# Kernel tuning notes

Measured on AMD Instinct MI355X. Metric: run time of the kernel, lower is better.

Reference implementation:

```python
import jax, jax.numpy as jnp
import numpy as np

NUM_HEADS = 16
ROPE_BASE = 10000.0


def _rope(q, k, seq_len, head_dim):
    # cos/sin: [S, D] -> broadcast over batch and heads via [:, None, :]
    inv_freq = 1.0 / (ROPE_BASE ** (jnp.arange(0, head_dim, 2, dtype=jnp.float32) / head_dim))
    t = jnp.arange(seq_len, dtype=jnp.float32)
    freqs = t[:, None] * inv_freq[None, :]            # [S, D/2]
    emb = jnp.concatenate((freqs, freqs), axis=-1)    # [S, D]
    cos = jnp.cos(emb)[:, None, :]                    # [S, 1, D]
    sin = jnp.sin(emb)[:, None, :]
    def rot(x):
        return jnp.stack([-x[..., 1::2], x[..., ::2]], axis=-1).reshape(x.shape)
    q = q * cos + rot(q) * sin
    k = k * cos + rot(k) * sin
    return q, k


def setup_inputs() -> dict:
    key = jax.random.key(0)
    ks = jax.random.split(key, 5)
    B, S, D = 2, 2048, 2048
    return {
        "hidden_states": jax.random.normal(ks[0], (B, S, D), dtype=jnp.float32),
        "Wq": jax.random.normal(ks[1], (D, D), dtype=jnp.float32) * 0.02,
        "Wk": jax.random.normal(ks[2], (D, D), dtype=jnp.float32) * 0.02,
        "Wv": jax.random.normal(ks[3], (D, D), dtype=jnp.float32) * 0.02,
        "Wo": jax.random.normal(ks[4], (D, D), dtype=jnp.float32) * 0.02,
        "attention_mask": jnp.ones((B, S), dtype=bool),
        "position_ids": S,  # passed to rotary as seq_len
    }


def reference(hidden_states, Wq, Wk, Wv, Wo, attention_mask, position_ids):
    B, S, D = hidden_states.shape
    H = NUM_HEADS
    hd = D // H
    q = (hidden_states @ Wq.T).reshape(B, S, H, hd)
    k = (hidden_states @ Wk.T).reshape(B, S, H, hd)
    v = (hidden_states @ Wv.T).reshape(B, S, H, hd)
    q, k = _rope(q, k, position_ids, hd)
    scores = jnp.einsum('bqhd,bkhd->bhqk', q, k) / jnp.sqrt(jnp.float32(hd))
    scores = jnp.where(attention_mask[:, None, None, :], scores, -jnp.inf)
    attn = jax.nn.softmax(scores, axis=-1)
    out = jnp.einsum('bhqk,bkhd->bqhd', attn, v).reshape(B, S, D)
    return out @ Wo.T
```

## Files before the change

kernel.cpp:

```cpp
#include <hip/hip_runtime.h>
#include <hip/hip_bf16.h>
#include <math.h>

typedef __hip_bfloat16 bf16;
typedef __attribute__((ext_vector_type(8))) short bf16x8;
typedef __attribute__((ext_vector_type(4))) float f32x4;

#define AS1 __attribute__((address_space(1)))
#define AS3 __attribute__((address_space(3)))

static constexpr int BATCH = 2, S = 2048, D = 2048, H = 16, HD = 128;
static constexpr int M = BATCH * S;
static constexpr float SCALE = 0.08838834764831845f;

__device__ __forceinline__ void gload_lds16(const void* g, void* l) {
  __builtin_amdgcn_global_load_lds((AS1 void*)g, (AS3 void*)l, 16, 0, 0);
}

__device__ __forceinline__ unsigned short f2bu(float f) {
  bf16 h = __float2bfloat16(f);
  return *reinterpret_cast<unsigned short*>(&h);
}

__global__ void cast_kernel(const float* __restrict__ in,
                            unsigned short* __restrict__ out, int n4) {
  int i = blockIdx.x * blockDim.x + threadIdx.x;
  int stride = gridDim.x * blockDim.x;
  for (; i < n4; i += stride) {
    float4 v = reinterpret_cast<const float4*>(in)[i];
    ushort4 o;
    o.x = f2bu(v.x); o.y = f2bu(v.y); o.z = f2bu(v.z); o.w = f2bu(v.w);
    reinterpret_cast<ushort4*>(out)[i] = o;
  }
}

__global__ void rope_tab_kernel(float2* __restrict__ cs) {
  int s = blockIdx.x, j = threadIdx.x;
  double inv = exp(-(double)j * 0.14391156831212793);
  float ang = (float)s * (float)inv;
  double da = (double)ang;
  cs[s * 64 + j] = make_float2((float)cos(da), (float)sin(da));
}

template <int EPI>
__global__ __launch_bounds__(256, 2) void gemm_bt(const bf16* __restrict__ A,
                                                  const bf16* __restrict__ B,
                                                  void* __restrict__ outp,
                                                  const float2* __restrict__ cs,
                                                  float oscale) {
  constexpr int K = 2048;
  __shared__ bf16 smA[2][128 * 32];
  __shared__ bf16 smB[2][128 * 32];
  const int tid = threadIdx.x;
  const int l = tid & 63, w = tid >> 6;
  const int wm = w >> 1, wn = w & 1;
  const int bm = blockIdx.y, bn = blockIdx.x;
  const int lr = l & 15, lg = l >> 4;

  f32x4 acc[4][4] = {};

  auto stage = [&](bf16* dst, const bf16* src, int row0, int k0) {
    #pragma unroll
    for (int i = 0; i < 2; ++i) {
      int idx = tid + i * 256;
      int row = idx >> 2, seg = idx & 3;
      gload_lds16(src + (size_t)(row0 + row) * K + k0 + seg * 8, dst + idx * 8);
    }
  };

  stage(smA[0], A, bm * 128, 0);
  stage(smB[0], B, bn * 128, 0);
  asm volatile("s_waitcnt vmcnt(0)" ::: "memory");
  __syncthreads();

  for (int kt = 0; kt < K / 32; ++kt) {
    const int cur = kt & 1;
    if (kt + 1 < K / 32) {
      stage(smA[cur ^ 1], A, bm * 128, (kt + 1) * 32);
      stage(smB[cur ^ 1], B, bn * 128, (kt + 1) * 32);
    }
    bf16x8 af[4], bfr[4];
    #pragma unroll
    for (int fm = 0; fm < 4; ++fm)
      af[fm] = *reinterpret_cast<const bf16x8*>(
          &smA[cur][(wm * 64 + fm * 16 + lr) * 32 + lg * 8]);
    #pragma unroll
    for (int fn = 0; fn < 4; ++fn)
      bfr[fn] = *reinterpret_cast<const bf16x8*>(
          &smB[cur][(wn * 64 + fn * 16 + lr) * 32 + lg * 8]);
    #pragma unroll
    for (int fm = 0; fm < 4; ++fm)
      #pragma unroll
      for (int fn = 0; fn < 4; ++fn)
        acc[fm][fn] = __builtin_amdgcn_mfma_f32_16x16x32_bf16(af[fm], bfr[fn],
                                                              acc[fm][fn], 0, 0, 0);
    __syncthreads();
  }

  const int row0 = bm * 128 + wm * 64 + lg * 4;
  const int col0 = bn * 128 + wn * 64 + lr;

  if constexpr (EPI == 0) {
    bf16* o = reinterpret_cast<bf16*>(outp);
    #pragma unroll
    for (int fm = 0; fm < 4; ++fm) {
      #pragma unroll
      for (int fn = 0; fn < 4; ++fn) {
        const int col = col0 + fn * 16;
        const int j = col & 63;
        const bool odd = (col & 1);
        #pragma unroll
        for (int r = 0; r < 4; ++r) {
          float v = acc[fm][fn][r];
          float p = __shfl_xor(v, 1);
          int row = row0 + fm * 16 + r;
          int s = row & (S - 1);
          float2 c = cs[s * 64 + j];
          float nv = (v * c.x + (odd ? p : -p) * c.y) * oscale;
          o[(size_t)row * D + col] = __float2bfloat16(nv);
        }
      }
    }
  } else if constexpr (EPI == 1) {
    bf16* o = reinterpret_cast<bf16*>(outp);
    #pragma unroll
    for (int fm = 0; fm < 4; ++fm) {
      #pragma unroll
      for (int fn = 0; fn < 4; ++fn) {
        int row = row0 + fm * 16;
        int col = col0 + fn * 16;
        int b_ = row >> 11, sp = row & (S - 1);
        int h = col >> 7, d = col & (HD - 1);
        size_t off = ((size_t)(b_ * H + h) * HD + d) * S + sp;
        ushort4 pk;
        pk.x = f2bu(acc[fm][fn][0]);
        pk.y = f2bu(acc[fm][fn][1]);
        pk.z = f2bu(acc[fm][fn][2]);
        pk.w = f2bu(acc[fm][fn][3]);
        *reinterpret_cast<ushort4*>(o + off) = pk;
      }
    }
  } else {
    float* o = reinterpret_cast<float*>(outp);
    #pragma unroll
    for (int fm = 0; fm < 4; ++fm)
      #pragma unroll
      for (int fn = 0; fn < 4; ++fn)
        #pragma unroll
        for (int r = 0; r < 4; ++r)
          o[(size_t)(row0 + fm * 16 + r) * D + col0 + fn * 16] = acc[fm][fn][r];
  }
}

__global__ __launch_bounds__(256, 2) void attn_kernel(const bf16* __restrict__ Q,
                                                      const bf16* __restrict__ Kmat,
                                                      const bf16* __restrict__ Vt,
                                                      bf16* __restrict__ O) {
  __shared__ bf16 kv_lds[2][16384];
  __shared__ bf16 plds[4][16][72];
  const int tid = threadIdx.x;
  const int l = tid & 63, w = tid >> 6;
  const int lr = l & 15, lg = l >> 4;
  const int bh = blockIdx.y;
  const int b = bh >> 4, h = bh & 15;
  const int q0 = blockIdx.x * 64 + w * 16;

  bf16x8 aq[4];
  #pragma unroll
  for (int ks = 0; ks < 4; ++ks)
    aq[ks] = *reinterpret_cast<const bf16x8*>(
        &Q[((size_t)b * S + q0 + lr) * D + h * HD + ks * 32 + lg * 8]);

  const bf16* ksrc[4];
  const bf16* vsrc[4];
  int kldsoff[4], vldsoff[4];
  #pragma unroll
  for (int i = 0; i < 4; ++i) {
    int idx = tid + i * 256;
    int krow = idx >> 4, kcb = (idx & 15) << 4;
    int kcol = (kcb ^ ((krow & 7) << 4)) >> 1;
    ksrc[i] = Kmat + ((size_t)b * S + krow) * D + h * HD + kcol;
    kldsoff[i] = idx * 8;
    int vrow = idx >> 3, vcb = (idx & 7) << 4;
    int vcol = (vcb ^ ((vrow & 7) << 4)) >> 1;
    vsrc[i] = Vt + ((size_t)bh * HD + vrow) * S + vcol;
    vldsoff[i] = 8192 + idx * 8;
  }

  auto stage = [&](int buf, int t) {
    #pragma unroll
    for (int i = 0; i < 4; ++i) {
      gload_lds16(ksrc[i] + (size_t)t * 64 * D, &kv_lds[buf][kldsoff[i]]);
      gload_lds16(vsrc[i] + t * 64, &kv_lds[buf][vldsoff[i]]);
    }
  };

  f32x4 oacc[8] = {};
  float m[4], ls[4];
  #pragma unroll
  for (int r = 0; r < 4; ++r) { m[r] = -1e30f; ls[r] = 0.f; }

  stage(0, 0);
  asm volatile("s_waitcnt vmcnt(0)" ::: "memory");
  __syncthreads();

  const int swz = (lr & 7) << 4;

  for (int t = 0; t < S / 64; ++t) {
    const int cur = t & 1;
    if (t + 1 < S / 64) stage(cur ^ 1, t + 1);
    const bf16* Kl = &kv_lds[cur][0];
    const bf16* Vl = &kv_lds[cur][8192];

    f32x4 sf[4] = {};
    __builtin_amdgcn_s_setprio(1);
    #pragma unroll
    for (int ksub = 0; ksub < 4; ++ksub) {
      #pragma unroll
      for (int ks = 0; ks < 4; ++ks) {
        bf16x8 bk = *reinterpret_cast<const bf16x8*>(
            &Kl[(ksub * 16 + lr) * 128 + (((ks * 64 + lg * 16) ^ swz) >> 1)]);
        sf[ksub] = __builtin_amdgcn_mfma_f32_16x16x32_bf16(aq[ks], bk, sf[ksub], 0, 0, 0);
      }
    }
    __builtin_amdgcn_s_setprio(0);

    #pragma unroll
    for (int r = 0; r < 4; ++r) {
      float mx = fmaxf(fmaxf(sf[0][r], sf[1][r]), fmaxf(sf[2][r], sf[3][r]));
      #pragma unroll
      for (int off = 1; off < 16; off <<= 1) mx = fmaxf(mx, __shfl_xor(mx, off));
      if (!__all(mx <= m[r] + 8.f)) {
        float mn = fmaxf(m[r], mx);
        float al = __expf(m[r] - mn);
        m[r] = mn;
        ls[r] *= al;
        #pragma unroll
        for (int df = 0; df < 8; ++df) oacc[df][r] *= al;
      }
      #pragma unroll
      for (int ksub = 0; ksub < 4; ++ksub) {
        float p = __expf(sf[ksub][r] - m[r]);
        ls[r] += p;
        plds[w][lg * 4 + r][ksub * 16 + lr] = __float2bfloat16(p);
      }
    }

    bf16x8 pa0 = *reinterpret_cast<const bf16x8*>(&plds[w][lr][lg * 8]);
    bf16x8 pa1 = *reinterpret_cast<const bf16x8*>(&plds[w][lr][32 + lg * 8]);
    __builtin_amdgcn_s_setprio(1);
    #pragma unroll
    for (int df = 0; df < 8; ++df) {
      const int vr = df * 16 + lr;
      bf16x8 bv0 = *reinterpret_cast<const bf16x8*>(
          &Vl[vr * 64 + (((lg * 16) ^ swz) >> 1)]);
      bf16x8 bv1 = *reinterpret_cast<const bf16x8*>(
          &Vl[vr * 64 + (((64 + lg * 16) ^ swz) >> 1)]);
      oacc[df] = __builtin_amdgcn_mfma_f32_16x16x32_bf16(pa0, bv0, oacc[df], 0, 0, 0);
      oacc[df] = __builtin_amdgcn_mfma_f32_16x16x32_bf16(pa1, bv1, oacc[df], 0, 0, 0);
    }
    __builtin_amdgcn_s_setprio(0);
    asm volatile("s_waitcnt vmcnt(0)" ::: "memory");
    __syncthreads();
  }

  #pragma unroll
  for (int r = 0; r < 4; ++r) {
    #pragma unroll
    for (int off = 1; off < 16; off <<= 1) ls[r] += __shfl_xor(ls[r], off);
    ls[r] = 1.0f / ls[r];
  }
  #pragma unroll
  for (int df = 0; df < 8; ++df) {
    #pragma unroll
    for (int r = 0; r < 4; ++r) {
      float v = oacc[df][r] * ls[r];
      O[((size_t)b * S + q0 + lg * 4 + r) * D + h * HD + df * 16 + lr] =
          __float2bfloat16(v);
    }
  }
}

extern "C" void kernel_launch(void* const* d_in, const int* in_sizes, int n_in,
                              void* d_out, int out_size, void* d_ws, size_t ws_size,
                              hipStream_t stream) {
  const float* hs = (const float*)d_in[0];
  const float* Wq = (const float*)d_in[1];
  const float* Wk = (const float*)d_in[2];
  const float* Wv = (const float*)d_in[3];
  const float* Wo = (const float*)d_in[4];
  float* out = (float*)d_out;

  const size_t nTok = (size_t)M * D;
  const size_t nW = (size_t)D * D;
  bf16* hsb = (bf16*)d_ws;
  bf16* wqb = hsb + nTok;
  bf16* wkb = wqb + nW;
  bf16* wvb = wkb + nW;
  bf16* wob = wvb + nW;
  bf16* qb  = wob + nW;
  bf16* kb  = qb + nTok;
  bf16* vtb = kb + nTok;
  bf16* ob  = vtb + nTok;
  float2* cs = (float2*)(ob + nTok);

  cast_kernel<<<2048, 256, 0, stream>>>(hs, (unsigned short*)hsb, (int)(nTok / 4));
  cast_kernel<<<1024, 256, 0, stream>>>(Wq, (unsigned short*)wqb, (int)(nW / 4));
  cast_kernel<<<1024, 256, 0, stream>>>(Wk, (unsigned short*)wkb, (int)(nW / 4));
  cast_kernel<<<1024, 256, 0, stream>>>(Wv, (unsigned short*)wvb, (int)(nW / 4));
  cast_kernel<<<1024, 256, 0, stream>>>(Wo, (unsigned short*)wob, (int)(nW / 4));
  rope_tab_kernel<<<S, 64, 0, stream>>>(cs);

  dim3 gg(D / 128, M / 128);
  gemm_bt<0><<<gg, 256, 0, stream>>>(hsb, wqb, qb, cs, SCALE);
  gemm_bt<0><<<gg, 256, 0, stream>>>(hsb, wkb, kb, cs, 1.0f);
  gemm_bt<1><<<gg, 256, 0, stream>>>(hsb, wvb, vtb, nullptr, 1.0f);

  attn_kernel<<<dim3(S / 64, BATCH * H), 256, 0, stream>>>(qb, kb, vtb, ob);

  gemm_bt<2><<<gg, 256, 0, stream>>>(ob, wob, out, nullptr, 1.0f);
}
```

Baseline: 499.4 us.

## Process 32 query rows per wave in attention and restructure K/V staging

Each wave now handles two 16-row query tiles, and each block covers 128 queries. K and V fragments loaded from LDS are therefore reused across twice as many MFMAs, and half as many blocks reload the same K/V tiles. The LDS plan changes to double-buffered K with a single V buffer. V for the current tile is issued first and waited on with a partial vmcnt before the PV stage, so the V load overlaps the QK and softmax work. The max-rescale check is merged into one wave vote across both tiles, which cuts shuffles. The cost is higher register pressure under launch_bounds(256,2) and fewer blocks in the grid (512), which may reduce occupancy or cause spills.

Measured after the change: 440.0 us. -11.9%, faster.

```diff
diff --git a/kernel.cpp b/kernel.cpp
--- a/kernel.cpp
+++ b/kernel.cpp
@@ -156,51 +156,48 @@
                                                       const bf16* __restrict__ Kmat,
                                                       const bf16* __restrict__ Vt,
                                                       bf16* __restrict__ O) {
-  __shared__ bf16 kv_lds[2][16384];
-  __shared__ bf16 plds[4][16][72];
+  __shared__ bf16 kv_lds[24576];
+  __shared__ bf16 plds[4][32][72];
   const int tid = threadIdx.x;
   const int l = tid & 63, w = tid >> 6;
   const int lr = l & 15, lg = l >> 4;
   const int bh = blockIdx.y;
   const int b = bh >> 4, h = bh & 15;
-  const int q0 = blockIdx.x * 64 + w * 16;
-
-  bf16x8 aq[4];
-  #pragma unroll
-  for (int ks = 0; ks < 4; ++ks)
-    aq[ks] = *reinterpret_cast<const bf16x8*>(
-        &Q[((size_t)b * S + q0 + lr) * D + h * HD + ks * 32 + lg * 8]);
+  const int q0 = blockIdx.x * 128 + w * 32;
+
+  bf16x8 aq[2][4];
+  #pragma unroll
+  for (int qs = 0; qs < 2; ++qs)
+    #pragma unroll
+    for (int ks = 0; ks < 4; ++ks)
+      aq[qs][ks] = *reinterpret_cast<const bf16x8*>(
+          &Q[((size_t)b * S + q0 + qs * 16 + lr) * D + h * HD + ks * 32 + lg * 8]);
 
   const bf16* ksrc[4];
   const bf16* vsrc[4];
-  int kldsoff[4], vldsoff[4];
+  int koff[4], voff[4];
   #pragma unroll
   for (int i = 0; i < 4; ++i) {
     int idx = tid + i * 256;
     int krow = idx >> 4, kcb = (idx & 15) << 4;
     int kcol = (kcb ^ ((krow & 7) << 4)) >> 1;
     ksrc[i] = Kmat + ((size_t)b * S + krow) * D + h * HD + kcol;
-    kldsoff[i] = idx * 8;
+    koff[i] = idx * 8;
     int vrow = idx >> 3, vcb = (idx & 7) << 4;
     int vcol = (vcb ^ ((vrow & 7) << 4)) >> 1;
     vsrc[i] = Vt + ((size_t)bh * HD + vrow) * S + vcol;
-    vldsoff[i] = 8192 + idx * 8;
-  }
-
-  auto stage = [&](int buf, int t) {
-    #pragma unroll
-    for (int i = 0; i < 4; ++i) {
-      gload_lds16(ksrc[i] + (size_t)t * 64 * D, &kv_lds[buf][kldsoff[i]]);
-      gload_lds16(vsrc[i] + t * 64, &kv_lds[buf][vldsoff[i]]);
-    }
-  };
-
-  f32x4 oacc[8] = {};
-  float m[4], ls[4];
-  #pragma unroll
-  for (int r = 0; r < 4; ++r) { m[r] = -1e30f; ls[r] = 0.f; }
-
-  stage(0, 0);
+    voff[i] = 16384 + idx * 8;
+  }
+
+  f32x4 oacc[2][8] = {};
+  float m[2][4], ls[2][4];
+  #pragma unroll
+  for (int qs = 0; qs < 2; ++qs)
+    #pragma unroll
+    for (int r = 0; r < 4; ++r) { m[qs][r] = -1e30f; ls[qs][r] = 0.f; }
+
+  #pragma unroll
+  for (int i = 0; i < 4; ++i) gload_lds16(ksrc[i], &kv_lds[koff[i]]);
   asm volatile("s_waitcnt vmcnt(0)" ::: "memory");
   __syncthreads();
 
@@ -208,46 +205,80 @@
 
   for (int t = 0; t < S / 64; ++t) {
     const int cur = t & 1;
-    if (t + 1 < S / 64) stage(cur ^ 1, t + 1);
-    const bf16* Kl = &kv_lds[cur][0];
-    const bf16* Vl = &kv_lds[cur][8192];
-
-    f32x4 sf[4] = {};
+    #pragma unroll
+    for (int i = 0; i < 4; ++i) gload_lds16(vsrc[i] + t * 64, &kv_lds[voff[i]]);
+    #pragma unroll
+    for (int i = 0; i < 4; ++i)
+      gload_lds16(ksrc[i] + (size_t)(t + 1) * 64 * D,
+                  &kv_lds[(cur ^ 1) * 8192 + koff[i]]);
+    const bf16* Kl = &kv_lds[cur * 8192];
+    const bf16* Vl = &kv_lds[16384];
+
+    f32x4 sf[2][4] = {};
     __builtin_amdgcn_s_setprio(1);
     #pragma unroll
     for (int ksub = 0; ksub < 4; ++ksub) {
-      #pragma unroll
-      for (int ks = 0; ks < 4; ++ks) {
-        bf16x8 bk = *reinterpret_cast<const bf16x8*>(
+      bf16x8 bk[4];
+      #pragma unroll
+      for (int ks = 0; ks < 4; ++ks)
+        bk[ks] = *reinterpret_cast<const bf16x8*>(
             &Kl[(ksub * 16 + lr) * 128 + (((ks * 64 + lg * 16) ^ swz) >> 1)]);
-        sf[ksub] = __builtin_amdgcn_mfma_f32_16x16x32_bf16(aq[ks], bk, sf[ksub], 0, 0, 0);
-      }
+      #pragma unroll
+      for (int qs = 0; qs < 2; ++qs)
+        #pragma unroll
+        for (int ks = 0; ks < 4; ++ks)
+          sf[qs][ksub] =
+              __builtin_amdgcn_mfma_f32_16x16x32_bf16(aq[qs][ks], bk[ks], sf[qs][ksub], 0, 0, 0);
     }
     __builtin_amdgcn_s_setprio(0);
 
-    #pragma unroll
-    for (int r = 0; r < 4; ++r) {
-      float mx = fmaxf(fmaxf(sf[0][r], sf[1][r]), fmaxf(sf[2][r], sf[3][r]));
-      #pragma unroll
-      for (int off = 1; off < 16; off <<= 1) mx = fmaxf(mx, __shfl_xor(mx, off));
-      if (!__all(mx <= m[r] + 8.f)) {
-        float mn = fmaxf(m[r], mx);
-        float al = __expf(m[r] - mn);
-        m[r] = mn;
-        ls[r] *= al;
-        #pragma unroll
-        for (int df = 0; df < 8; ++df) oacc[df][r] *= al;
-      }
-      #pragma unroll
-      for (int ksub = 0; ksub < 4; ++ksub) {
-        float p = __expf(sf[ksub][r] - m[r]);
-        ls[r] += p;
-        plds[w][lg * 4 + r][ksub * 16 + lr] = __float2bfloat16(p);
-      }
-    }
-
-    bf16x8 pa0 = *reinterpret_cast<const bf16x8*>(&plds[w][lr][lg * 8]);
-    bf16x8 pa1 = *reinterpret_cast<const bf16x8*>(&plds[w][lr][32 + lg * 8]);
+    float lmx[2][4];
+    int ok = 1;
+    #pragma unroll
+    for (int qs = 0; qs < 2; ++qs)
+      #pragma unroll
+      for (int r = 0; r < 4; ++r) {
+        lmx[qs][r] = fmaxf(fmaxf(sf[qs][0][r], sf[qs][1][r]),
+                           fmaxf(sf[qs][2][r], sf[qs][3][r]));
+        ok &= (lmx[qs][r] <= m[qs][r] + 8.f);
+      }
+    if (!__all(ok)) {
+      #pragma unroll
+      for (int qs = 0; qs < 2; ++qs)
+        #pragma unroll
+        for (int r = 0; r < 4; ++r) {
+          float mxf = lmx[qs][r];
+          #pragma unroll
+          for (int off = 1; off < 16; off <<= 1) mxf = fmaxf(mxf, __shfl_xor(mxf, off));
+          float mn = fmaxf(m[qs][r], mxf);
+          float al = __expf(m[qs][r] - mn);
+          m[qs][r] = mn;
+          ls[qs][r] *= al;
+          #pragma unroll
+          for (int df = 0; df < 8; ++df) oacc[qs][df][r] *= al;
+        }
+    }
+    #pragma unroll
+    for (int qs = 0; qs < 2; ++qs)
+      #pragma unroll
+      for (int ksub = 0; ksub < 4; ++ksub)
+        #pragma unroll
+        for (int r = 0; r < 4; ++r) {
+          float p = __expf(sf[qs][ksub][r] - m[qs][r]);
+          ls[qs][r] += p;
+          plds[w][qs * 16 + lg * 4 + r][ksub * 16 + lr] = __float2bfloat16(p);
+        }
+
+    asm volatile("s_waitcnt vmcnt(4)" ::: "memory");
+    __builtin_amdgcn_s_barrier();
+
+    bf16x8 pa[2][2];
+    #pragma unroll
+    for (int qs = 0; qs < 2; ++qs)
+      #pragma unroll
+      for (int hh = 0; hh < 2; ++hh)
+        pa[qs][hh] = *reinterpret_cast<const bf16x8*>(
+            &plds[w][qs * 16 + lr][hh * 32 + lg * 8]);
     __builtin_amdgcn_s_setprio(1);
     #pragma unroll
     for (int df = 0; df < 8; ++df) {
@@ -256,29 +287,36 @@
           &Vl[vr * 64 + (((lg * 16) ^ swz) >> 1)]);
       bf16x8 bv1 = *reinterpret_cast<const bf16x8*>(
           &Vl[vr * 64 + (((64 + lg * 16) ^ swz) >> 1)]);
-      oacc[df] = __builtin_amdgcn_mfma_f32_16x16x32_bf16(pa0, bv0, oacc[df], 0, 0, 0);
-      oacc[df] = __builtin_amdgcn_mfma_f32_16x16x32_bf16(pa1, bv1, oacc[df], 0, 0, 0);
+      #pragma unroll
+      for (int qs = 0; qs < 2; ++qs) {
+        oacc[qs][df] = __builtin_amdgcn_mfma_f32_16x16x32_bf16(pa[qs][0], bv0, oacc[qs][df], 0, 0, 0);
+        oacc[qs][df] = __builtin_amdgcn_mfma_f32_16x16x32_bf16(pa[qs][1], bv1, oacc[qs][df], 0, 0, 0);
+      }
     }
     __builtin_amdgcn_s_setprio(0);
+
     asm volatile("s_waitcnt vmcnt(0)" ::: "memory");
-    __syncthreads();
-  }
-
-  #pragma unroll
-  for (int r = 0; r < 4; ++r) {
-    #pragma unroll
-    for (int off = 1; off < 16; off <<= 1) ls[r] += __shfl_xor(ls[r], off);
-    ls[r] = 1.0f / ls[r];
-  }
-  #pragma unroll
-  for (int df = 0; df < 8; ++df) {
+    __builtin_amdgcn_s_barrier();
+  }
+
+  #pragma unroll
+  for (int qs = 0; qs < 2; ++qs)
     #pragma unroll
     for (int r = 0; r < 4; ++r) {
-      float v = oacc[df][r] * ls[r];
-      O[((size_t)b * S + q0 + lg * 4 + r) * D + h * HD + df * 16 + lr] =
-          __float2bfloat16(v);
-    }
-  }
+      #pragma unroll
+      for (int off = 1; off < 16; off <<= 1) ls[qs][r] += __shfl_xor(ls[qs][r], off);
+      ls[qs][r] = 1.0f / ls[qs][r];
+    }
+  #pragma unroll
+  for (int qs = 0; qs < 2; ++qs)
+    #pragma unroll
+    for (int df = 0; df < 8; ++df)
+      #pragma unroll
+      for (int r = 0; r < 4; ++r) {
+        float v = oacc[qs][df][r] * ls[qs][r];
+        O[((size_t)b * S + q0 + qs * 16 + lg * 4 + r) * D + h * HD + df * 16 + lr] =
+            __float2bfloat16(v);
+      }
 }
 
 extern "C" void kernel_launch(void* const* d_in, const int* in_sizes, int n_in,
@@ -316,7 +354,7 @@
   gemm_bt<0><<<gg, 256, 0, stream>>>(hsb, wkb, kb, cs, 1.0f);
   gemm_bt<1><<<gg, 256, 0, stream>>>(hsb, wvb, vtb, nullptr, 1.0f);
 
-  attn_kernel<<<dim3(S / 64, BATCH * H), 256, 0, stream>>>(qb, kb, vtb, ob);
+  attn_kernel<<<dim3(S / 128, BATCH * H), 256, 0, stream>>>(qb, kb, vtb, ob);
 
   gemm_bt<2><<<gg, 256, 0, stream>>>(ob, wob, out, nullptr, 1.0f);
 }
```
